# Performance work log

Hardware: AMD Instinct MI355X
Metric: run time of the kernel (lower is better)

Reference implementation:

```python
import jax, jax.numpy as jnp
import numpy as np

MARGIN = 0.3
N, D = 8192, 128
NUM_CLASSES = 512


def setup_inputs() -> dict:
    key = jax.random.key(0)
    k1, k2 = jax.random.split(key)
    embeddings = jax.random.normal(k1, (N, D), dtype=jnp.float32)
    targets = jax.random.randint(k2, (N,), 0, NUM_CLASSES, dtype=jnp.int64)
    return {"embeddings": embeddings, "targets": targets}


def reference(embeddings, targets):
    x = embeddings.astype(jnp.float32)
    # pairwise squared-euclidean: ||xi||^2 + ||xj||^2 - 2 xi.xj, clamped then sqrt
    sq = jnp.sum(x * x, axis=1)  # [N]
    dist = sq[:, None] + sq[None, :] - 2.0 * (x @ x.T)
    dist = jnp.sqrt(jnp.clip(dist, 1e-12, None))  # [N, N]

    is_pos = targets[:, None] == targets[None, :]  # includes diagonal, as in torch code

    # batch-hard mining: per-row hardest positive (max) and hardest negative (min)
    dist_ap = jnp.max(jnp.where(is_pos, dist, -jnp.inf), axis=1)
    dist_an = jnp.min(jnp.where(is_pos, jnp.inf, dist), axis=1)

    # MarginRankingLoss(margin)(dist_an, dist_ap, y=1) = mean(relu(margin - (dist_an - dist_ap)))
    loss = jnp.mean(jax.nn.relu(dist_ap - dist_an + MARGIN))
    return loss
```

## Files before the change

### kernel.cpp

```cpp
#include <hip/hip_runtime.h>
#include <hip/hip_bf16.h>

#define N_ROWS 8192
#define DIM 128
#define MARGIN_F 0.3f

typedef __attribute__((ext_vector_type(8))) short short8;
typedef __attribute__((ext_vector_type(4))) float f32x4;
typedef __attribute__((ext_vector_type(4))) int int4v;

__global__ __launch_bounds__(256) void prep_kernel(
    const float* __restrict__ x, const int* __restrict__ tgt,
    unsigned short* __restrict__ xbB, float2* __restrict__ meta,
    int* __restrict__ apb, int* __restrict__ anb) {
  const int w = threadIdx.x >> 6, l = threadIdx.x & 63;
  const int row = blockIdx.x * 4 + w;
  float2 v = reinterpret_cast<const float2*>(x + (size_t)row * DIM)[l];
  __hip_bfloat16 b0 = __float2bfloat16(v.x);
  __hip_bfloat16 b1 = __float2bfloat16(v.y);
  ushort2 st;
  st.x = *reinterpret_cast<unsigned short*>(&b0);
  st.y = *reinterpret_cast<unsigned short*>(&b1);
  const int c16 = row >> 4, l15r = row & 15;
  const int unit = c16 * 256 + (l >> 4) * 64 + ((l >> 2) & 3) * 16 + l15r;
  reinterpret_cast<ushort2*>(xbB)[unit * 4 + (l & 3)] = st;

  float s = v.x * v.x + v.y * v.y;
  #pragma unroll
  for (int off = 32; off >= 1; off >>= 1) s += __shfl_xor(s, off);
  if (l == 0) {
    float2 m;
    m.x = s;
    m.y = __int_as_float(tgt[row]);
    meta[row] = m;
    apb[row] = 0x00000000;
    anb[row] = 0x7f800000;
  }
}

__global__ __launch_bounds__(256, 4) void gram_mine_kernel(
    const unsigned short* __restrict__ xbB, const float2* __restrict__ meta,
    int* __restrict__ apb, int* __restrict__ anb) {
  const int t = threadIdx.x;
  const int w = t >> 6, l = t & 63;
  const int l15 = l & 15, l4 = l >> 4;
  const int rb = blockIdx.x * 128 + w * 32;
  const int chunkbase = blockIdx.y * 512;

  const short8* xf = reinterpret_cast<const short8*>(xbB);

  short8 a[2][4];
  #pragma unroll
  for (int rf = 0; rf < 2; ++rf)
    #pragma unroll
    for (int kk = 0; kk < 4; ++kk)
      a[rf][kk] = xf[(rb >> 4 << 8) + rf * 256 + kk * 64 + l];

  int t_r[8];
  #pragma unroll
  for (int rf = 0; rf < 2; ++rf)
    #pragma unroll
    for (int rg = 0; rg < 4; ++rg)
      t_r[rf * 4 + rg] = __float_as_int(meta[rb + rf * 16 + l4 * 4 + rg].y);

  float ap2[8], an2[8];
  #pragma unroll
  for (int i = 0; i < 8; ++i) { ap2[i] = -__builtin_inff(); an2[i] = __builtin_inff(); }

  for (int ct = 0; ct < 8; ++ct) {
    const int colbase = chunkbase + ct * 64;
    const int cb16 = colbase >> 4;

    float sqc[4]; int tc[4];
    #pragma unroll
    for (int cf = 0; cf < 4; ++cf) {
      float2 m = meta[colbase + cf * 16 + l15];
      sqc[cf] = m.x; tc[cf] = __float_as_int(m.y);
    }

    f32x4 acc[2][4];
    #pragma unroll
    for (int rf = 0; rf < 2; ++rf)
      #pragma unroll
      for (int cf = 0; cf < 4; ++cf) acc[rf][cf] = (f32x4){0.f, 0.f, 0.f, 0.f};

    #pragma unroll
    for (int kk = 0; kk < 4; ++kk) {
      #pragma unroll
      for (int cf = 0; cf < 4; ++cf) {
        short8 b = xf[(cb16 + cf) * 256 + kk * 64 + l];
        acc[0][cf] = __builtin_amdgcn_mfma_f32_16x16x32_bf16(a[0][kk], b, acc[0][cf], 0, 0, 0);
        acc[1][cf] = __builtin_amdgcn_mfma_f32_16x16x32_bf16(a[1][kk], b, acc[1][cf], 0, 0, 0);
      }
    }

    #pragma unroll
    for (int cf = 0; cf < 4; ++cf) {
      #pragma unroll
      for (int rf = 0; rf < 2; ++rf)
        #pragma unroll
        for (int rg = 0; rg < 4; ++rg) {
          int idx = rf * 4 + rg;
          float v = fmaf(-2.f, acc[rf][cf][rg], sqc[cf]);
          bool pos = (t_r[idx] == tc[cf]);
          ap2[idx] = pos ? fmaxf(ap2[idx], v) : ap2[idx];
          an2[idx] = pos ? an2[idx] : fminf(an2[idx], v);
        }
    }
  }

  #pragma unroll
  for (int i = 0; i < 8; ++i) {
    #pragma unroll
    for (int off = 1; off < 16; off <<= 1) {
      ap2[i] = fmaxf(ap2[i], __shfl_xor(ap2[i], off));
      an2[i] = fminf(an2[i], __shfl_xor(an2[i], off));
    }
  }
  if (l15 == 0) {
    #pragma unroll
    for (int rf = 0; rf < 2; ++rf)
      #pragma unroll
      for (int rg = 0; rg < 4; ++rg) {
        int row = rb + rf * 16 + l4 * 4 + rg;
        float sqr = meta[row].x;
        float a2 = fmaxf(ap2[rf * 4 + rg] + sqr, 1e-12f);
        float n2 = fmaxf(an2[rf * 4 + rg] + sqr, 1e-12f);
        atomicMax(apb + row, __float_as_int(a2));
        atomicMin(anb + row, __float_as_int(n2));
      }
  }
}

__global__ __launch_bounds__(1024) void loss_kernel(
    const int4v* __restrict__ apb, const int4v* __restrict__ anb,
    float* __restrict__ out) {
  __shared__ float red[16];
  float s = 0.f;
  for (int i = threadIdx.x; i < N_ROWS / 4; i += 1024) {
    int4v a4 = apb[i], n4 = anb[i];
    #pragma unroll
    for (int j = 0; j < 4; ++j) {
      float ap = sqrtf(__int_as_float(a4[j]));
      float an = sqrtf(__int_as_float(n4[j]));
      float li = ap - an + MARGIN_F;
      s += li > 0.f ? li : 0.f;
    }
  }
  #pragma unroll
  for (int off = 32; off >= 1; off >>= 1) s += __shfl_xor(s, off);
  const int w = threadIdx.x >> 6, l = threadIdx.x & 63;
  if (l == 0) red[w] = s;
  __syncthreads();
  if (threadIdx.x < 16) {
    float v = red[threadIdx.x];
    #pragma unroll
    for (int off = 8; off >= 1; off >>= 1) v += __shfl_xor(v, off);
    if (threadIdx.x == 0) out[0] = v / (float)N_ROWS;
  }
}

extern "C" void kernel_launch(void* const* d_in, const int* in_sizes, int n_in,
                              void* d_out, int out_size, void* d_ws, size_t ws_size,
                              hipStream_t stream) {
  const float* x = (const float*)d_in[0];
  const int* tgt = (const int*)d_in[1];
  float* out = (float*)d_out;

  char* ws = (char*)d_ws;
  unsigned short* xbB = (unsigned short*)ws;
  float2* meta = (float2*)(ws + 2097152);
  int* apb = (int*)(ws + 2097152 + 65536);
  int* anb = (int*)(ws + 2097152 + 65536 + 32768);

  prep_kernel<<<2048, 256, 0, stream>>>(x, tgt, xbB, meta, apb, anb);
  gram_mine_kernel<<<dim3(64, 16), 256, 0, stream>>>(xbB, meta, apb, anb);
  loss_kernel<<<1, 1024, 0, stream>>>((const int4v*)apb, (const int4v*)anb, out);
}
```

Before: 51.30 us.

## Sort rows by class to skip positive-mask checks on clean tiles

Adds a histogram/prefix-sum kernel and a ballot-based scatter kernel that reorder rows by target class, then builds the bf16 Gram layout in sorted order. In the mining kernel, a column tile whose class range does not overlap the row block's class range is known to be all negatives, so it takes a cheap min-only path with no per-element label comparisons. This removes compare/select work and the per-tile label loads from most tiles, at the cost of two extra small kernel launches, a gathered read in prep, and a serial single-block histogram.

```diff
diff --git a/kernel.cpp b/kernel.cpp
--- a/kernel.cpp
+++ b/kernel.cpp
@@ -3,25 +3,68 @@
 
 #define N_ROWS 8192
 #define DIM 128
+#define NUM_CLS 512
 #define MARGIN_F 0.3f
 
 typedef __attribute__((ext_vector_type(8))) short short8;
 typedef __attribute__((ext_vector_type(4))) float f32x4;
 typedef __attribute__((ext_vector_type(4))) int int4v;
 
+__global__ __launch_bounds__(512) void hist_kernel(
+    const int* __restrict__ tgt, int* __restrict__ class_start) {
+  __shared__ int h[NUM_CLS];
+  const int t = threadIdx.x;
+  h[t] = 0;
+  __syncthreads();
+  for (int i = t; i < N_ROWS; i += 512) atomicAdd(&h[tgt[i]], 1);
+  __syncthreads();
+  int own = h[t];
+  int incl = own;
+  #pragma unroll
+  for (int off = 1; off < NUM_CLS; off <<= 1) {
+    int v = (t >= off) ? h[t - off] : 0;
+    __syncthreads();
+    incl += v;
+    h[t] = incl;
+    __syncthreads();
+  }
+  class_start[t] = incl - own;
+}
+
+__global__ __launch_bounds__(256) void scatter_kernel(
+    const int* __restrict__ tgt, const int* __restrict__ class_start,
+    int* __restrict__ sorted_row, int* __restrict__ cls) {
+  const int c = blockIdx.x * 4 + (threadIdx.x >> 6);
+  const int l = threadIdx.x & 63;
+  const int base = class_start[c];
+  int cnt = 0;
+  for (int i0 = 0; i0 < N_ROWS; i0 += 64) {
+    int ti = tgt[i0 + l];
+    unsigned long long m = __ballot(ti == c);
+    if (ti == c) {
+      int rank = __popcll(m & ((1ull << l) - 1ull));
+      int pos = base + cnt + rank;
+      sorted_row[pos] = i0 + l;
+      cls[pos] = c;
+    }
+    cnt += __popcll(m);
+  }
+}
+
 __global__ __launch_bounds__(256) void prep_kernel(
-    const float* __restrict__ x, const int* __restrict__ tgt,
-    unsigned short* __restrict__ xbB, float2* __restrict__ meta,
+    const float* __restrict__ x, const int* __restrict__ sorted_row,
+    unsigned short* __restrict__ xbB, float* __restrict__ sqv,
     int* __restrict__ apb, int* __restrict__ anb) {
   const int w = threadIdx.x >> 6, l = threadIdx.x & 63;
-  const int row = blockIdx.x * 4 + w;
+  const int j = blockIdx.x * 4 + w;
+  const int row = sorted_row[j];
   float2 v = reinterpret_cast<const float2*>(x + (size_t)row * DIM)[l];
   __hip_bfloat16 b0 = __float2bfloat16(v.x);
   __hip_bfloat16 b1 = __float2bfloat16(v.y);
   ushort2 st;
   st.x = *reinterpret_cast<unsigned short*>(&b0);
   st.y = *reinterpret_cast<unsigned short*>(&b1);
-  const int c16 = row >> 4, l15r = row & 15;
+  const int c16 = j >> 4, l15r = j & 15;
   const int unit = c16 * 256 + (l >> 4) * 64 + ((l >> 2) & 3) * 16 + l15r;
   reinterpret_cast<ushort2*>(xbB)[unit * 4 + (l & 3)] = st;
 
@@ -29,18 +72,15 @@
   #pragma unroll
   for (int off = 32; off >= 1; off >>= 1) s += __shfl_xor(s, off);
   if (l == 0) {
-    float2 m;
-    m.x = s;
-    m.y = __int_as_float(tgt[row]);
-    meta[row] = m;
-    apb[row] = 0x00000000;
-    anb[row] = 0x7f800000;
+    sqv[j] = s;
+    apb[j] = 0x00000000;
+    anb[j] = 0x7f800000;
   }
 }
 
 __global__ __launch_bounds__(256, 4) void gram_mine_kernel(
-    const unsigned short* __restrict__ xbB, const float2* __restrict__ meta,
-    int* __restrict__ apb, int* __restrict__ anb) {
+    const unsigned short* __restrict__ xbB, const float* __restrict__ sqv,
+    const int* __restrict__ cls, int* __restrict__ apb, int* __restrict__ anb) {
   const int t = threadIdx.x;
   const int w = t >> 6, l = t & 63;
   const int l15 = l & 15, l4 = l >> 4;
@@ -56,12 +96,14 @@
     for (int kk = 0; kk < 4; ++kk)
       a[rf][kk] = xf[(rb >> 4 << 8) + rf * 256 + kk * 64 + l];
 
+  const int rcl_lo = cls[rb], rcl_hi = cls[rb + 31];
+
   int t_r[8];
   #pragma unroll
   for (int rf = 0; rf < 2; ++rf)
     #pragma unroll
     for (int rg = 0; rg < 4; ++rg)
-      t_r[rf * 4 + rg] = __float_as_int(meta[rb + rf * 16 + l4 * 4 + rg].y);
+      t_r[rf * 4 + rg] = cls[rb + rf * 16 + l4 * 4 + rg];
 
   float ap2[8], an2[8];
   #pragma unroll
@@ -71,12 +113,11 @@
     const int colbase = chunkbase + ct * 64;
     const int cb16 = colbase >> 4;
 
-    float sqc[4]; int tc[4];
-    #pragma unroll
-    for (int cf = 0; cf < 4; ++cf) {
-      float2 m = meta[colbase + cf * 16 + l15];
-      sqc[cf] = m.x; tc[cf] = __float_as_int(m.y);
-    }
+    float sqc[4];
+    #pragma unroll
+    for (int cf = 0; cf < 4; ++cf) sqc[cf] = sqv[colbase + cf * 16 + l15];
+    const int ccl_lo = cls[colbase], ccl_hi = cls[colbase + 63];
+    const bool clean = (ccl_hi < rcl_lo) || (ccl_lo > rcl_hi);
 
     f32x4 acc[2][4];
     #pragma unroll
@@ -94,18 +135,35 @@
       }
     }
 
-    #pragma unroll
-    for (int cf = 0; cf < 4; ++cf) {
+    if (clean) {
       #pragma unroll
       for (int rf = 0; rf < 2; ++rf)
         #pragma unroll
         for (int rg = 0; rg < 4; ++rg) {
           int idx = rf * 4 + rg;
-          float v = fmaf(-2.f, acc[rf][cf][rg], sqc[cf]);
-          bool pos = (t_r[idx] == tc[cf]);
-          ap2[idx] = pos ? fmaxf(ap2[idx], v) : ap2[idx];
-          an2[idx] = pos ? an2[idx] : fminf(an2[idx], v);
+          float v0 = fmaf(-2.f, acc[rf][0][rg], sqc[0]);
+          float v1 = fmaf(-2.f, acc[rf][1][rg], sqc[1]);
+          float v2 = fmaf(-2.f, acc[rf][2][rg], sqc[2]);
+          float v3 = fmaf(-2.f, acc[rf][3][rg], sqc[3]);
+          an2[idx] = fminf(fminf(fminf(v0, v1), fminf(v2, v3)), an2[idx]);
         }
+    } else {
+      int tc[4];
+      #pragma unroll
+      for (int cf = 0; cf < 4; ++cf) tc[cf] = cls[colbase + cf * 16 + l15];
+      #pragma unroll
+      for (int cf = 0; cf < 4; ++cf) {
+        #pragma unroll
+        for (int rf = 0; rf < 2; ++rf)
+          #pragma unroll
+          for (int rg = 0; rg < 4; ++rg) {
+            int idx = rf * 4 + rg;
+            float v = fmaf(-2.f, acc[rf][cf][rg], sqc[cf]);
+            bool pos = (t_r[idx] == tc[cf]);
+            ap2[idx] = pos ? fmaxf(ap2[idx], v) : ap2[idx];
+            an2[idx] = pos ? an2[idx] : fminf(an2[idx], v);
+          }
+      }
     }
   }
 
@@ -123,7 +181,7 @@
       #pragma unroll
       for (int rg = 0; rg < 4; ++rg) {
         int row = rb + rf * 16 + l4 * 4 + rg;
-        float sqr = meta[row].x;
+        float sqr = sqv[row];
         float a2 = fmaxf(ap2[rf * 4 + rg] + sqr, 1e-12f);
         float n2 = fmaxf(an2[rf * 4 + rg] + sqr, 1e-12f);
         atomicMax(apb + row, __float_as_int(a2));
@@ -169,11 +227,16 @@
 
   char* ws = (char*)d_ws;
   unsigned short* xbB = (unsigned short*)ws;
-  float2* meta = (float2*)(ws + 2097152);
+  float* sqv = (float*)(ws + 2097152);
+  int* cls = (int*)(ws + 2097152 + 32768);
   int* apb = (int*)(ws + 2097152 + 65536);
-  int* anb = (int*)(ws + 2097152 + 65536 + 32768);
-
-  prep_kernel<<<2048, 256, 0, stream>>>(x, tgt, xbB, meta, apb, anb);
-  gram_mine_kernel<<<dim3(64, 16), 256, 0, stream>>>(xbB, meta, apb, anb);
+  int* anb = (int*)(ws + 2097152 + 98304);
+  int* sorted_row = (int*)(ws + 2097152 + 131072);
+  int* class_start = (int*)(ws + 2097152 + 163840);
+
+  hist_kernel<<<1, 512, 0, stream>>>(tgt, class_start);
+  scatter_kernel<<<128, 256, 0, stream>>>(tgt, class_start, sorted_row, cls);
+  prep_kernel<<<2048, 256, 0, stream>>>(x, sorted_row, xbB, sqv, apb, anb);
+  gram_mine_kernel<<<dim3(64, 16), 256, 0, stream>>>(xbB, sqv, cls, apb, anb);
   loss_kernel<<<1, 1024, 0, stream>>>((const int4v*)apb, (const int4v*)anb, out);
 }
```

Result: slower. 66.93 us (+30.5%).

## Software-pipeline B-fragment loads and split column chunks across more blocks

Applied to the files above, without the earlier changes.

Register double-buffering prefetches the next k-slice of B fragments and the next tile's metadata while the MFMAs of the current slice run, hiding global-load latency. The column chunk per block is halved (4 tiles instead of 8) and the grid doubled to 64x32, giving more blocks and parallelism. The cost is twice as many atomic min/max updates. Launch bounds drop from 4 to 3 waves per SIMD to make room for the extra registers, which lowers occupancy.

```diff
diff --git a/kernel.cpp b/kernel.cpp
--- a/kernel.cpp
+++ b/kernel.cpp
@@ -38,23 +38,23 @@
   }
 }
 
-__global__ __launch_bounds__(256, 4) void gram_mine_kernel(
+__global__ __launch_bounds__(256, 3) void gram_mine_kernel(
     const unsigned short* __restrict__ xbB, const float2* __restrict__ meta,
     int* __restrict__ apb, int* __restrict__ anb) {
   const int t = threadIdx.x;
   const int w = t >> 6, l = t & 63;
   const int l15 = l & 15, l4 = l >> 4;
   const int rb = blockIdx.x * 128 + w * 32;
-  const int chunkbase = blockIdx.y * 512;
+  const int chunk = blockIdx.y * 256;
 
   const short8* xf = reinterpret_cast<const short8*>(xbB);
 
-  short8 a[2][4];
-  #pragma unroll
-  for (int rf = 0; rf < 2; ++rf)
-    #pragma unroll
-    for (int kk = 0; kk < 4; ++kk)
-      a[rf][kk] = xf[(rb >> 4 << 8) + rf * 256 + kk * 64 + l];
+  short8 a0[4], a1[4];
+  #pragma unroll
+  for (int kk = 0; kk < 4; ++kk) {
+    a0[kk] = xf[(rb >> 4) * 256 + kk * 64 + l];
+    a1[kk] = xf[((rb >> 4) + 1) * 256 + kk * 64 + l];
+  }
 
   int t_r[8];
   #pragma unroll
@@ -67,46 +67,68 @@
   #pragma unroll
   for (int i = 0; i < 8; ++i) { ap2[i] = -__builtin_inff(); an2[i] = __builtin_inff(); }
 
-  for (int ct = 0; ct < 8; ++ct) {
-    const int colbase = chunkbase + ct * 64;
-    const int cb16 = colbase >> 4;
-
-    float sqc[4]; int tc[4];
+  short8 bb[2][4];
+  float2 mc[4];
+  const int cb0 = chunk >> 4;
+  #pragma unroll
+  for (int cf = 0; cf < 4; ++cf) {
+    bb[0][cf] = xf[(cb0 + cf) * 256 + l];
+    mc[cf] = meta[chunk + cf * 16 + l15];
+  }
+
+  #pragma unroll
+  for (int ct = 0; ct < 4; ++ct) {
+    const int cb16 = (chunk >> 4) + ct * 4;
+    const int nt = (ct < 3) ? (ct + 1) : 3;
+    const int nb16 = (chunk >> 4) + nt * 4;
+
+    f32x4 acc[2][4];
+    #pragma unroll
+    for (int rf = 0; rf < 2; ++rf)
+      #pragma unroll
+      for (int cf = 0; cf < 4; ++cf) acc[rf][cf] = (f32x4){0.f, 0.f, 0.f, 0.f};
+
+    float2 mn[4];
+    #pragma unroll
+    for (int kk = 0; kk < 4; ++kk) {
+      if (kk < 3) {
+        #pragma unroll
+        for (int cf = 0; cf < 4; ++cf)
+          bb[(kk + 1) & 1][cf] = xf[(cb16 + cf) * 256 + (kk + 1) * 64 + l];
+      } else {
+        #pragma unroll
+        for (int cf = 0; cf < 4; ++cf)
+          bb[0][cf] = xf[(nb16 + cf) * 256 + l];
+        #pragma unroll
+        for (int cf = 0; cf < 4; ++cf)
+          mn[cf] = meta[chunk + nt * 64 + cf * 16 + l15];
+      }
+      #pragma unroll
+      for (int cf = 0; cf < 4; ++cf) {
+        acc[0][cf] = __builtin_amdgcn_mfma_f32_16x16x32_bf16(
+            a0[kk], bb[kk & 1][cf], acc[0][cf], 0, 0, 0);
+        acc[1][cf] = __builtin_amdgcn_mfma_f32_16x16x32_bf16(
+            a1[kk], bb[kk & 1][cf], acc[1][cf], 0, 0, 0);
+      }
+    }
+
     #pragma unroll
     for (int cf = 0; cf < 4; ++cf) {
-      float2 m = meta[colbase + cf * 16 + l15];
-      sqc[cf] = m.x; tc[cf] = __float_as_int(m.y);
-    }
-
-    f32x4 acc[2][4];
-    #pragma unroll
-    for (int rf = 0; rf < 2; ++rf)
-      #pragma unroll
-      for (int cf = 0; cf < 4; ++cf) acc[rf][cf] = (f32x4){0.f, 0.f, 0.f, 0.f};
-
-    #pragma unroll
-    for (int kk = 0; kk < 4; ++kk) {
-      #pragma unroll
-      for (int cf = 0; cf < 4; ++cf) {
-        short8 b = xf[(cb16 + cf) * 256 + kk * 64 + l];
-        acc[0][cf] = __builtin_amdgcn_mfma_f32_16x16x32_bf16(a[0][kk], b, acc[0][cf], 0, 0, 0);
-        acc[1][cf] = __builtin_amdgcn_mfma_f32_16x16x32_bf16(a[1][kk], b, acc[1][cf], 0, 0, 0);
-      }
-    }
-
-    #pragma unroll
-    for (int cf = 0; cf < 4; ++cf) {
+      const float sqc = mc[cf].x;
+      const int tc = __float_as_int(mc[cf].y);
       #pragma unroll
       for (int rf = 0; rf < 2; ++rf)
         #pragma unroll
         for (int rg = 0; rg < 4; ++rg) {
           int idx = rf * 4 + rg;
-          float v = fmaf(-2.f, acc[rf][cf][rg], sqc[cf]);
-          bool pos = (t_r[idx] == tc[cf]);
+          float v = fmaf(-2.f, acc[rf][cf][rg], sqc);
+          bool pos = (t_r[idx] == tc);
           ap2[idx] = pos ? fmaxf(ap2[idx], v) : ap2[idx];
           an2[idx] = pos ? an2[idx] : fminf(an2[idx], v);
         }
     }
+    #pragma unroll
+    for (int cf = 0; cf < 4; ++cf) mc[cf] = mn[cf];
   }
 
   #pragma unroll
@@ -174,6 +196,6 @@
   int* anb = (int*)(ws + 2097152 + 65536 + 32768);
 
   prep_kernel<<<2048, 256, 0, stream>>>(x, tgt, xbB, meta, apb, anb);
-  gram_mine_kernel<<<dim3(64, 16), 256, 0, stream>>>(xbB, meta, apb, anb);
+  gram_mine_kernel<<<dim3(64, 32), 256, 0, stream>>>(xbB, meta, apb, anb);
   loss_kernel<<<1, 1024, 0, stream>>>((const int4v*)apb, (const int4v*)anb, out);
 }
```

Result: faster. 48.66 us (-5.1%).

## Software-pipeline gram tiles with prefetch and fold -2 and column norm into MFMA

Applied to the files above, without the earlier changes.

The gram/mining kernel is restructured into a double-buffered software pipeline. The next 32-column B tile and its metadata are prefetched into registers while the current tile's MFMAs run and the previous tile's epilogue executes. A second bf16 copy of the embeddings pre-scaled by -2 is written in prep, and the accumulator is seeded with the column squared norm, which removes the per-element fma. The grid is halved to 8 column chunks of 1024 with launch bounds lowered to 2 waves per SIMD, trading occupancy and extra workspace and prep writes for more latency hiding and fewer atomics. Pre-scaling by -2 before bf16 rounding is exact, so precision is unchanged.

```diff
diff --git a/kernel.cpp b/kernel.cpp
--- a/kernel.cpp
+++ b/kernel.cpp
@@ -11,19 +11,24 @@
 
 __global__ __launch_bounds__(256) void prep_kernel(
     const float* __restrict__ x, const int* __restrict__ tgt,
-    unsigned short* __restrict__ xbB, float2* __restrict__ meta,
-    int* __restrict__ apb, int* __restrict__ anb) {
+    unsigned short* __restrict__ xbA, unsigned short* __restrict__ xbB,
+    float2* __restrict__ meta, int* __restrict__ apb, int* __restrict__ anb) {
   const int w = threadIdx.x >> 6, l = threadIdx.x & 63;
   const int row = blockIdx.x * 4 + w;
   float2 v = reinterpret_cast<const float2*>(x + (size_t)row * DIM)[l];
   __hip_bfloat16 b0 = __float2bfloat16(v.x);
   __hip_bfloat16 b1 = __float2bfloat16(v.y);
-  ushort2 st;
-  st.x = *reinterpret_cast<unsigned short*>(&b0);
-  st.y = *reinterpret_cast<unsigned short*>(&b1);
+  __hip_bfloat16 a0 = __float2bfloat16(-2.f * v.x);
+  __hip_bfloat16 a1 = __float2bfloat16(-2.f * v.y);
+  ushort2 stB, stA;
+  stB.x = *reinterpret_cast<unsigned short*>(&b0);
+  stB.y = *reinterpret_cast<unsigned short*>(&b1);
+  stA.x = *reinterpret_cast<unsigned short*>(&a0);
+  stA.y = *reinterpret_cast<unsigned short*>(&a1);
   const int c16 = row >> 4, l15r = row & 15;
   const int unit = c16 * 256 + (l >> 4) * 64 + ((l >> 2) & 3) * 16 + l15r;
-  reinterpret_cast<ushort2*>(xbB)[unit * 4 + (l & 3)] = st;
+  reinterpret_cast<ushort2*>(xbB)[unit * 4 + (l & 3)] = stB;
+  reinterpret_cast<ushort2*>(xbA)[unit * 4 + (l & 3)] = stA;
 
   float s = v.x * v.x + v.y * v.y;
   #pragma unroll
@@ -38,23 +43,25 @@
   }
 }
 
-__global__ __launch_bounds__(256, 4) void gram_mine_kernel(
-    const unsigned short* __restrict__ xbB, const float2* __restrict__ meta,
-    int* __restrict__ apb, int* __restrict__ anb) {
+__global__ __launch_bounds__(256, 2) void gram_mine_kernel(
+    const unsigned short* __restrict__ xbA, const unsigned short* __restrict__ xbB,
+    const float2* __restrict__ meta, int* __restrict__ apb, int* __restrict__ anb) {
   const int t = threadIdx.x;
   const int w = t >> 6, l = t & 63;
   const int l15 = l & 15, l4 = l >> 4;
   const int rb = blockIdx.x * 128 + w * 32;
-  const int chunkbase = blockIdx.y * 512;
-
-  const short8* xf = reinterpret_cast<const short8*>(xbB);
-
-  short8 a[2][4];
-  #pragma unroll
-  for (int rf = 0; rf < 2; ++rf)
-    #pragma unroll
-    for (int kk = 0; kk < 4; ++kk)
-      a[rf][kk] = xf[(rb >> 4 << 8) + rf * 256 + kk * 64 + l];
+  const int chunk = blockIdx.y * 1024;
+  const int chunkb = chunk >> 4;
+
+  const short8* xfA = reinterpret_cast<const short8*>(xbA);
+  const short8* xfB = reinterpret_cast<const short8*>(xbB);
+
+  short8 a0[4], a1[4];
+  #pragma unroll
+  for (int kk = 0; kk < 4; ++kk) {
+    a0[kk] = xfA[(rb >> 4) * 256 + kk * 64 + l];
+    a1[kk] = xfA[((rb >> 4) + 1) * 256 + kk * 64 + l];
+  }
 
   int t_r[8];
   #pragma unroll
@@ -67,47 +74,69 @@
   #pragma unroll
   for (int i = 0; i < 8; ++i) { ap2[i] = -__builtin_inff(); an2[i] = __builtin_inff(); }
 
-  for (int ct = 0; ct < 8; ++ct) {
-    const int colbase = chunkbase + ct * 64;
-    const int cb16 = colbase >> 4;
-
-    float sqc[4]; int tc[4];
-    #pragma unroll
-    for (int cf = 0; cf < 4; ++cf) {
-      float2 m = meta[colbase + cf * 16 + l15];
-      sqc[cf] = m.x; tc[cf] = __float_as_int(m.y);
-    }
-
-    f32x4 acc[2][4];
-    #pragma unroll
-    for (int rf = 0; rf < 2; ++rf)
-      #pragma unroll
-      for (int cf = 0; cf < 4; ++cf) acc[rf][cf] = (f32x4){0.f, 0.f, 0.f, 0.f};
-
-    #pragma unroll
-    for (int kk = 0; kk < 4; ++kk) {
-      #pragma unroll
-      for (int cf = 0; cf < 4; ++cf) {
-        short8 b = xf[(cb16 + cf) * 256 + kk * 64 + l];
-        acc[0][cf] = __builtin_amdgcn_mfma_f32_16x16x32_bf16(a[0][kk], b, acc[0][cf], 0, 0, 0);
-        acc[1][cf] = __builtin_amdgcn_mfma_f32_16x16x32_bf16(a[1][kk], b, acc[1][cf], 0, 0, 0);
-      }
-    }
-
-    #pragma unroll
-    for (int cf = 0; cf < 4; ++cf) {
-      #pragma unroll
-      for (int rf = 0; rf < 2; ++rf)
-        #pragma unroll
-        for (int rg = 0; rg < 4; ++rg) {
-          int idx = rf * 4 + rg;
-          float v = fmaf(-2.f, acc[rf][cf][rg], sqc[cf]);
-          bool pos = (t_r[idx] == tc[cf]);
-          ap2[idx] = pos ? fmaxf(ap2[idx], v) : ap2[idx];
-          an2[idx] = pos ? an2[idx] : fminf(an2[idx], v);
-        }
-    }
-  }
+  short8 bb0[8], bb1[8];
+  float2 mc0[2], mc1[2];
+  f32x4 accA[2][2], accB[2][2];
+
+#define PREF_B(IDX, BB) do {                                                  \
+    const int cb16_ = chunkb + (IDX) * 2;                                     \
+    _Pragma("unroll")                                                         \
+    for (int kk_ = 0; kk_ < 4; ++kk_) {                                       \
+      BB[kk_ * 2 + 0] = xfB[(cb16_ + 0) * 256 + kk_ * 64 + l];                \
+      BB[kk_ * 2 + 1] = xfB[(cb16_ + 1) * 256 + kk_ * 64 + l];                \
+    } } while (0)
+
+#define META_L(IDX, MC) do {                                                  \
+    MC[0] = meta[chunk + (IDX) * 32 + l15];                                   \
+    MC[1] = meta[chunk + (IDX) * 32 + 16 + l15];  } while (0)
+
+#define MFMA_T(BB, MC, ACC) do {                                              \
+    _Pragma("unroll")                                                         \
+    for (int cf_ = 0; cf_ < 2; ++cf_) {                                       \
+      float s_ = MC[cf_].x;                                                   \
+      f32x4 ci_ = {s_, s_, s_, s_};                                           \
+      ACC[0][cf_] = ci_; ACC[1][cf_] = ci_;                                   \
+    }                                                                         \
+    _Pragma("unroll")                                                         \
+    for (int kk_ = 0; kk_ < 4; ++kk_) {                                       \
+      _Pragma("unroll")                                                       \
+      for (int cf_ = 0; cf_ < 2; ++cf_) {                                     \
+        ACC[0][cf_] = __builtin_amdgcn_mfma_f32_16x16x32_bf16(                \
+            a0[kk_], BB[kk_ * 2 + cf_], ACC[0][cf_], 0, 0, 0);                \
+        ACC[1][cf_] = __builtin_amdgcn_mfma_f32_16x16x32_bf16(                \
+            a1[kk_], BB[kk_ * 2 + cf_], ACC[1][cf_], 0, 0, 0);                \
+      } } } while (0)
+
+#define EPI_T(ACC, MC) do {                                                   \
+    _Pragma("unroll")                                                         \
+    for (int cf_ = 0; cf_ < 2; ++cf_) {                                       \
+      const int tc_ = __float_as_int(MC[cf_].y);                              \
+      _Pragma("unroll")                                                       \
+      for (int rf_ = 0; rf_ < 2; ++rf_) {                                     \
+        _Pragma("unroll")                                                     \
+        for (int rg_ = 0; rg_ < 4; ++rg_) {                                   \
+          const int ix_ = rf_ * 4 + rg_;                                      \
+          float v_ = ACC[rf_][cf_][rg_];                                      \
+          bool p_ = (t_r[ix_] == tc_);                                        \
+          ap2[ix_] = p_ ? fmaxf(ap2[ix_], v_) : ap2[ix_];                     \
+          an2[ix_] = p_ ? an2[ix_] : fminf(an2[ix_], v_);                     \
+        } } } } while (0)
+
+  PREF_B(0, bb0); META_L(0, mc0);
+  MFMA_T(bb0, mc0, accA); PREF_B(1, bb1); META_L(1, mc1);
+
+  #pragma unroll 1
+  for (int p = 0; p < 15; ++p) {
+    const int o = 2 * p + 1;
+    MFMA_T(bb1, mc1, accB); PREF_B(o + 1, bb0); EPI_T(accA, mc0); META_L(o + 1, mc0);
+    MFMA_T(bb0, mc0, accA); PREF_B(o + 2, bb1); EPI_T(accB, mc1); META_L(o + 2, mc1);
+  }
+  MFMA_T(bb1, mc1, accB); EPI_T(accA, mc0); EPI_T(accB, mc1);
+
+#undef PREF_B
+#undef META_L
+#undef MFMA_T
+#undef EPI_T
 
   #pragma unroll
   for (int i = 0; i < 8; ++i) {
@@ -168,12 +197,13 @@
   float* out = (float*)d_out;
 
   char* ws = (char*)d_ws;
-  unsigned short* xbB = (unsigned short*)ws;
-  float2* meta = (float2*)(ws + 2097152);
-  int* apb = (int*)(ws + 2097152 + 65536);
-  int* anb = (int*)(ws + 2097152 + 65536 + 32768);
-
-  prep_kernel<<<2048, 256, 0, stream>>>(x, tgt, xbB, meta, apb, anb);
-  gram_mine_kernel<<<dim3(64, 16), 256, 0, stream>>>(xbB, meta, apb, anb);
+  unsigned short* xbA = (unsigned short*)ws;
+  unsigned short* xbB = (unsigned short*)(ws + 2097152);
+  float2* meta = (float2*)(ws + 4194304);
+  int* apb = (int*)(ws + 4194304 + 65536);
+  int* anb = (int*)(ws + 4194304 + 65536 + 32768);
+
+  prep_kernel<<<2048, 256, 0, stream>>>(x, tgt, xbA, xbB, meta, apb, anb);
+  gram_mine_kernel<<<dim3(64, 8), 256, 0, stream>>>(xbA, xbB, meta, apb, anb);
   loss_kernel<<<1, 1024, 0, stream>>>((const int4v*)apb, (const int4v*)anb, out);
 }
```

New measurement: 44.28 us. 13.7% less time.
